# Performance work log

Hardware: AMD Instinct MI355X
Metric: run time of the kernel (lower is better)

Reference implementation:

```python
import jax, jax.numpy as jnp
import numpy as np

B, S, D = 2, 2048, 2048
NH, NKV, HD = 16, 4, 128
ROPE_BASE = 10000.0
NEG = -1e9


def _rope_tables(seq_len, dim):
    inv_freq = 1.0 / ROPE_BASE ** (jnp.arange(0, dim, 2, dtype=jnp.float32) / dim)
    t = jnp.arange(seq_len, dtype=jnp.float32)
    freqs = jnp.outer(t, inv_freq)                      # [S, dim/2]
    return jnp.cos(freqs), jnp.sin(freqs)


def _apply_rope(x, cos, sin):
    # x: [B, S, H, HD]; interleaved-pair rotation matching the original module
    x1 = x[..., ::2]
    x2 = x[..., 1::2]
    c = cos[None, :, None, :]
    s = sin[None, :, None, :]
    out1 = x1 * c - x2 * s
    out2 = x1 * s + x2 * c
    return jnp.stack([out1, out2], axis=-1).reshape(x.shape)


def setup_inputs() -> dict:
    key = jax.random.key(0)
    ks = jax.random.split(key, 5)
    x = jax.random.normal(ks[0], (B, S, D), dtype=jnp.float32)
    # causal additive mask [1, 1, S, S]
    causal = jnp.tril(jnp.ones((S, S), dtype=jnp.bool_))
    mask = jnp.where(causal, 0.0, NEG).astype(jnp.float32)[None, None]
    Wq = jax.random.normal(ks[1], (D, NH * HD), dtype=jnp.float32) * (D ** -0.5)
    Wk = jax.random.normal(ks[2], (D, NKV * HD), dtype=jnp.float32) * (D ** -0.5)
    Wv = jax.random.normal(ks[3], (D, NKV * HD), dtype=jnp.float32) * (D ** -0.5)
    Wo = jax.random.normal(ks[4], (NH * HD, D), dtype=jnp.float32) * ((NH * HD) ** -0.5)
    return {"x": x, "mask": mask, "Wq": Wq, "Wk": Wk, "Wv": Wv, "Wo": Wo}


def reference(x, mask, Wq, Wk, Wv, Wo):
    b, s, _ = x.shape
    q = (x @ Wq).reshape(b, s, NH, HD)
    k = (x @ Wk).reshape(b, s, NKV, HD)
    v = (x @ Wv).reshape(b, s, NKV, HD)

    cos, sin = _rope_tables(s, HD)
    q = _apply_rope(q, cos, sin)
    k = _apply_rope(k, cos, sin)

    rep = NH // NKV
    k = jnp.repeat(k, rep, axis=2)                       # [b, s, NH, HD]
    v = jnp.repeat(v, rep, axis=2)

    q = q.transpose(0, 2, 1, 3)                          # [b, NH, s, HD]
    k = k.transpose(0, 2, 1, 3)
    v = v.transpose(0, 2, 1, 3)

    scores = jnp.einsum('bhqd,bhkd->bhqk', q, k) / jnp.sqrt(jnp.float32(HD))
    scores = scores + mask
    attn = jax.nn.softmax(scores, axis=-1)
    out = jnp.einsum('bhqk,bhkd->bhqd', attn, v)
    out = out.transpose(0, 2, 1, 3).reshape(b, s, NH * HD)
    return out @ Wo
```

## Files before the change

kernel.cpp:

```cpp
#include <hip/hip_runtime.h>
#include <stdint.h>

#define B_    2
#define S_    2048
#define D_    2048
#define NH_   16
#define NKV_  4
#define HD_   128
#define M_    (B_*S_)
#define NQKV_ 3072

typedef __bf16 bf16x8 __attribute__((ext_vector_type(8)));
typedef float  f32x4  __attribute__((ext_vector_type(4)));

__device__ __forceinline__ unsigned short f2bf(float f) {
    unsigned int u = __float_as_uint(f);
    u += 0x7fffu + ((u >> 16) & 1u);
    return (unsigned short)(u >> 16);
}

__device__ __forceinline__ void async_cp16(const unsigned short* g, unsigned short* l) {
    __builtin_amdgcn_global_load_lds((const __attribute__((address_space(1))) void*)g,
                                     (__attribute__((address_space(3))) void*)l, 16, 0, 0);
}

__global__ void cast_x(const float* __restrict__ x, unsigned short* __restrict__ xb) {
    int idx = blockIdx.x * 256 + threadIdx.x;
    float4 v = ((const float4*)x)[idx];
    unsigned int lo = (unsigned int)f2bf(v.x) | ((unsigned int)f2bf(v.y) << 16);
    unsigned int hi = (unsigned int)f2bf(v.z) | ((unsigned int)f2bf(v.w) << 16);
    ((uint2*)xb)[idx] = make_uint2(lo, hi);
}

__global__ void transpose_cast(const float* __restrict__ src,
                               unsigned short* __restrict__ dst, int ncols) {
    __shared__ float tile[32][33];
    int tx = threadIdx.x, ty = threadIdx.y;
    int n0 = blockIdx.x * 32, k0 = blockIdx.y * 32;
#pragma unroll
    for (int i = 0; i < 4; i++) {
        int k = k0 + ty + i * 8;
        tile[ty + i * 8][tx] = src[(long)k * ncols + n0 + tx];
    }
    __syncthreads();
#pragma unroll
    for (int i = 0; i < 4; i++) {
        int n = n0 + ty + i * 8;
        dst[(long)n * 2048 + k0 + tx] = f2bf(tile[tx][ty + i * 8]);
    }
}

__global__ __launch_bounds__(256) void gemm_bt(const unsigned short* __restrict__ A,
                                               const unsigned short* __restrict__ Bt,
                                               float* __restrict__ C, int N, int K) {
    __shared__ unsigned short As[128 * 32];
    __shared__ unsigned short Bs[128 * 32];
    const int tid  = threadIdx.x;
    const int lane = tid & 63, wid = tid >> 6;
    const int quad = lane >> 4, l16 = lane & 15;
    const int wm = wid >> 1, wn = wid & 1;
    const int m0 = blockIdx.y * 128, n0 = blockIdx.x * 128;
    f32x4 acc[4][4] = {};

    for (int k0 = 0; k0 < K; k0 += 32) {
        __syncthreads();
#pragma unroll
        for (int i = 0; i < 2; i++) {
            int gbase = (wid * 2 + i) * 64;
            int g = gbase + lane;
            int row = g >> 2, c = (g & 3) * 8;
            async_cp16(&A[(long)(m0 + row) * K + k0 + c], &As[gbase * 8]);
            async_cp16(&Bt[(long)(n0 + row) * K + k0 + c], &Bs[gbase * 8]);
        }
        __syncthreads();
        bf16x8 af[4], bfr[4];
#pragma unroll
        for (int mt = 0; mt < 4; mt++)
            af[mt] = *(const bf16x8*)&As[(wm * 64 + mt * 16 + l16) * 32 + quad * 8];
#pragma unroll
        for (int nt = 0; nt < 4; nt++)
            bfr[nt] = *(const bf16x8*)&Bs[(wn * 64 + nt * 16 + l16) * 32 + quad * 8];
#pragma unroll
        for (int mt = 0; mt < 4; mt++)
#pragma unroll
            for (int nt = 0; nt < 4; nt++)
                acc[mt][nt] = __builtin_amdgcn_mfma_f32_16x16x32_bf16(af[mt], bfr[nt], acc[mt][nt], 0, 0, 0);
    }
#pragma unroll
    for (int mt = 0; mt < 4; mt++)
#pragma unroll
        for (int nt = 0; nt < 4; nt++)
#pragma unroll
            for (int r = 0; r < 4; r++) {
                long row = m0 + wm * 64 + mt * 16 + quad * 4 + r;
                long col = n0 + wn * 64 + nt * 16 + l16;
                C[row * N + col] = acc[mt][nt][r];
            }
}

__global__ void rope_q(const float* __restrict__ qkv, unsigned short* __restrict__ Qr) {
    int gid = blockIdx.x * 256 + threadIdx.x;
    int p = gid & 63;  int t1 = gid >> 6;
    int h = t1 & 15;   int t2 = t1 >> 4;
    int s = t2 & 2047; int b = t2 >> 11;
    float2 xv = *(const float2*)&qkv[(long)(b * 2048 + s) * 3072 + h * 128 + 2 * p];
    float inv = exp2f(-(float)p * 0.20762050593046014f);
    float ang = (float)s * inv;
    float sn, cs; sincosf(ang, &sn, &cs);
    float o0 = xv.x * cs - xv.y * sn;
    float o1 = xv.x * sn + xv.y * cs;
    unsigned int pk = (unsigned int)f2bf(o0) | ((unsigned int)f2bf(o1) << 16);
    *(unsigned int*)&Qr[(((long)(b * 16 + h) * 2048 + s) * 128) + 2 * p] = pk;
}

__global__ void rope_k(const float* __restrict__ qkv, unsigned short* __restrict__ Kr) {
    int gid = blockIdx.x * 256 + threadIdx.x;
    int p = gid & 63;  int t1 = gid >> 6;
    int kvh = t1 & 3;  int t2 = t1 >> 2;
    int s = t2 & 2047; int b = t2 >> 11;
    float2 xv = *(const float2*)&qkv[(long)(b * 2048 + s) * 3072 + 2048 + kvh * 128 + 2 * p];
    float inv = exp2f(-(float)p * 0.20762050593046014f);
    float ang = (float)s * inv;
    float sn, cs; sincosf(ang, &sn, &cs);
    float o0 = xv.x * cs - xv.y * sn;
    float o1 = xv.x * sn + xv.y * cs;
    unsigned int pk = (unsigned int)f2bf(o0) | ((unsigned int)f2bf(o1) << 16);
    *(unsigned int*)&Kr[(((long)(b * 4 + kvh) * 2048 + s) * 128) + 2 * p] = pk;
}

__global__ void v_trans(const float* __restrict__ qkv, unsigned short* __restrict__ Vt) {
    __shared__ float tile[32][33];
    int tx = threadIdx.x, ty = threadIdx.y;
    int s0 = blockIdx.x * 32, d0 = blockIdx.y * 32;
    int bz = blockIdx.z;
    int b = bz >> 2, kvh = bz & 3;
#pragma unroll
    for (int i = 0; i < 4; i++) {
        int s = s0 + ty + i * 8;
        tile[ty + i * 8][tx] = qkv[(long)(b * 2048 + s) * 3072 + 2560 + kvh * 128 + d0 + tx];
    }
    __syncthreads();
#pragma unroll
    for (int i = 0; i < 4; i++) {
        int d = d0 + ty + i * 8;
        Vt[((long)bz * 128 + d) * 2048 + s0 + tx] = f2bf(tile[tx][ty + i * 8]);
    }
}

__global__ __launch_bounds__(256) void attn_fwd(const unsigned short* __restrict__ Qr,
                                                const unsigned short* __restrict__ Kr,
                                                const unsigned short* __restrict__ Vt,
                                                unsigned short* __restrict__ O) {
    __shared__ unsigned short Ks[64][136];
    __shared__ unsigned short Vs[128][72];
    __shared__ unsigned short Ps[4][16][72];
    const int tid  = threadIdx.x;
    const int lane = tid & 63, wid = tid >> 6;
    const int quad = lane >> 4, l16 = lane & 15;
    const int pid = blockIdx.x, h = blockIdx.y, b = blockIdx.z;
    const int kvh = h >> 2;
    const unsigned short* qp = Qr + (long)(b * NH_ + h) * S_ * HD_;
    const unsigned short* kp = Kr + (long)(b * NKV_ + kvh) * S_ * HD_;
    const unsigned short* vp = Vt + (long)(b * NKV_ + kvh) * HD_ * S_;
    const float sc2 = 0.08838834764831845f * 1.4426950408889634f;

    for (int phase = 0; phase < 2; phase++) {
        const int qt = phase ? pid : 31 - pid;
        const int qw = qt * 64 + wid * 16;

        bf16x8 aq[4];
#pragma unroll
        for (int ks = 0; ks < 4; ks++)
            aq[ks] = *(const bf16x8*)&qp[(long)(qw + l16) * HD_ + ks * 32 + quad * 8];

        f32x4 o[8] = {};
        float mi[4], li[4];
#pragma unroll
        for (int r = 0; r < 4; r++) { mi[r] = -3.0e38f; li[r] = 0.f; }

        for (int kt = 0; kt <= qt; kt++) {
            const int kv0 = kt * 64;
            __syncthreads();
#pragma unroll
            for (int i = 0; i < 4; i++) {
                int idx = tid + i * 256;
                int row = idx >> 4, c = (idx & 15) * 8;
                *(uint4*)&Ks[row][c] = *(const uint4*)&kp[(long)(kv0 + row) * HD_ + c];
            }
#pragma unroll
            for (int i = 0; i < 4; i++) {
                int idx = tid + i * 256;
                int hd = idx >> 3, c = (idx & 7) * 8;
                *(uint4*)&Vs[hd][c] = *(const uint4*)&vp[(long)hd * S_ + kv0 + c];
            }
            __syncthreads();

            f32x4 s[4] = {};
#pragma unroll
            for (int ks = 0; ks < 4; ks++)
#pragma unroll
                for (int nt = 0; nt < 4; nt++) {
                    bf16x8 kb = *(const bf16x8*)&Ks[nt * 16 + l16][ks * 32 + quad * 8];
                    s[nt] = __builtin_amdgcn_mfma_f32_16x16x32_bf16(aq[ks], kb, s[nt], 0, 0, 0);
                }

            float mt[4];
#pragma unroll
            for (int r = 0; r < 4; r++) mt[r] = -3.0e38f;
            if (kv0 + 63 > qw) {
#pragma unroll
                for (int nt = 0; nt < 4; nt++) {
                    int kvp = kv0 + nt * 16 + l16;
#pragma unroll
                    for (int r = 0; r < 4; r++) {
                        float sv = s[nt][r] * sc2;
                        sv = (kvp <= qw + quad * 4 + r) ? sv : -1.0e30f;
                        s[nt][r] = sv;
                        mt[r] = fmaxf(mt[r], sv);
                    }
                }
            } else {
#pragma unroll
                for (int nt = 0; nt < 4; nt++)
#pragma unroll
                    for (int r = 0; r < 4; r++) {
                        float sv = s[nt][r] * sc2;
                        s[nt][r] = sv;
                        mt[r] = fmaxf(mt[r], sv);
                    }
            }
#pragma unroll
            for (int off = 1; off < 16; off <<= 1)
#pragma unroll
                for (int r = 0; r < 4; r++)
                    mt[r] = fmaxf(mt[r], __shfl_xor(mt[r], off));
            float al[4], rs[4];
#pragma unroll
            for (int r = 0; r < 4; r++) {
                float mn = fmaxf(mi[r], mt[r]);
                al[r] = exp2f(mi[r] - mn);
                mi[r] = mn;
                rs[r] = 0.f;
            }
#pragma unroll
            for (int nt = 0; nt < 4; nt++)
#pragma unroll
                for (int r = 0; r < 4; r++) {
                    float pv = exp2f(s[nt][r] - mi[r]);
                    s[nt][r] = pv;
                    rs[r] += pv;
                }
#pragma unroll
            for (int off = 1; off < 16; off <<= 1)
#pragma unroll
                for (int r = 0; r < 4; r++)
                    rs[r] += __shfl_xor(rs[r], off);
#pragma unroll
            for (int r = 0; r < 4; r++) li[r] = li[r] * al[r] + rs[r];
#pragma unroll
            for (int t = 0; t < 8; t++)
#pragma unroll
                for (int r = 0; r < 4; r++) o[t][r] *= al[r];

#pragma unroll
            for (int nt = 0; nt < 4; nt++)
#pragma unroll
                for (int r = 0; r < 4; r++)
                    Ps[wid][quad * 4 + r][nt * 16 + l16] = f2bf(s[nt][r]);

#pragma unroll
            for (int ks2 = 0; ks2 < 2; ks2++) {
                bf16x8 pa = *(const bf16x8*)&Ps[wid][l16][ks2 * 32 + quad * 8];
#pragma unroll
                for (int vt = 0; vt < 8; vt++) {
                    bf16x8 vb = *(const bf16x8*)&Vs[vt * 16 + l16][ks2 * 32 + quad * 8];
                    o[vt] = __builtin_amdgcn_mfma_f32_16x16x32_bf16(pa, vb, o[vt], 0, 0, 0);
                }
            }
        }

#pragma unroll
        for (int r = 0; r < 4; r++) {
            float inv_l = 1.0f / li[r];
            int qpos = qw + quad * 4 + r;
#pragma unroll
            for (int vt = 0; vt < 8; vt++) {
                float val = o[vt][r] * inv_l;
                O[(long)(b * S_ + qpos) * 2048 + h * 128 + vt * 16 + l16] = f2bf(val);
            }
        }
    }
}

extern "C" void kernel_launch(void* const* d_in, const int* in_sizes, int n_in,
                              void* d_out, int out_size, void* d_ws, size_t ws_size,
                              hipStream_t stream) {
    const float* x  = (const float*)d_in[0];
    const float* Wq = (const float*)d_in[2];
    const float* Wk = (const float*)d_in[3];
    const float* Wv = (const float*)d_in[4];
    const float* Wo = (const float*)d_in[5];

    char* ws = (char*)d_ws;
    unsigned short* xb    = (unsigned short*)(ws);
    unsigned short* Wqkvt = (unsigned short*)(ws + 16777216);
    unsigned short* Wot   = (unsigned short*)(ws + 29360128);
    float*          qkv   = (float*)         (ws + 37748736);
    unsigned short* Qr    = (unsigned short*)(ws + 88080384);
    unsigned short* Kr    = (unsigned short*)(ws + 104857600);
    unsigned short* Vt    = (unsigned short*)(ws + 109051904);
    unsigned short* attn  = (unsigned short*)(ws + 113246208);

    cast_x<<<8192, 256, 0, stream>>>(x, xb);
    dim3 tb(32, 8);
    transpose_cast<<<dim3(64, 64), tb, 0, stream>>>(Wq, Wqkvt, 2048);
    transpose_cast<<<dim3(16, 64), tb, 0, stream>>>(Wk, Wqkvt + 2048 * 2048, 512);
    transpose_cast<<<dim3(16, 64), tb, 0, stream>>>(Wv, Wqkvt + 2560 * 2048, 512);
    transpose_cast<<<dim3(64, 64), tb, 0, stream>>>(Wo, Wot, 2048);

    gemm_bt<<<dim3(NQKV_ / 128, M_ / 128), 256, 0, stream>>>(xb, Wqkvt, qkv, NQKV_, D_);

    rope_q<<<16384, 256, 0, stream>>>(qkv, Qr);
    rope_k<<<4096, 256, 0, stream>>>(qkv, Kr);
    v_trans<<<dim3(64, 4, 8), tb, 0, stream>>>(qkv, Vt);

    attn_fwd<<<dim3(16, NH_, B_), 256, 0, stream>>>(Qr, Kr, Vt, attn);

    gemm_bt<<<dim3(D_ / 128, M_ / 128), 256, 0, stream>>>(attn, Wot, (float*)d_out, D_, NH_ * HD_);
}
```

Before: 386.9 us.

## Fuse RoPE and bf16 output into QKV GEMM epilogue, remap grids per XCD

The QKV GEMM epilogue now applies RoPE, using a precomputed cos/sin table and a lane shuffle, and writes bf16 Q/K directly. V is written as a bf16 row-major buffer that a bf16 transpose then reorders. This removes the fp32 qkv intermediate and the separate rope kernels. Both GEMMs use a 1D grid with block-to-tile remapping so adjacent N tiles land on the same XCD for L2 reuse. Attention drops its two-phase paired-tile scheme for one query tile per block on a doubled grid, which trades explicit causal load balancing for more blocks.

```diff
diff --git a/kernel.cpp b/kernel.cpp
--- a/kernel.cpp
+++ b/kernel.cpp
@@ -50,16 +50,33 @@
     }
 }
 
-__global__ __launch_bounds__(256) void gemm_bt(const unsigned short* __restrict__ A,
-                                               const unsigned short* __restrict__ Bt,
-                                               float* __restrict__ C, int N, int K) {
+__global__ void rope_tables(float2* __restrict__ ctab) {
+    int gid = blockIdx.x * 256 + threadIdx.x;
+    int s = gid >> 6, i = gid & 63;
+    float inv = exp2f(-(float)i * 0.20762050593046014f);
+    float ang = (float)s * inv;
+    float sn, cs; sincosf(ang, &sn, &cs);
+    ctab[gid] = make_float2(cs, sn);
+}
+
+__global__ __launch_bounds__(256) void gemm_qkv(const unsigned short* __restrict__ A,
+                                                const unsigned short* __restrict__ Bt,
+                                                const float2* __restrict__ ctab,
+                                                unsigned short* __restrict__ Qr,
+                                                unsigned short* __restrict__ Kr,
+                                                unsigned short* __restrict__ Vrow) {
     __shared__ unsigned short As[128 * 32];
     __shared__ unsigned short Bs[128 * 32];
+    const int K = D_, N = NQKV_;
+    const int bid = blockIdx.x;
+    const int xcd = bid & 7, ii = bid >> 3;
+    const int bx = xcd * 3 + (ii % 3);
+    const int by = ii / 3;
     const int tid  = threadIdx.x;
     const int lane = tid & 63, wid = tid >> 6;
     const int quad = lane >> 4, l16 = lane & 15;
     const int wm = wid >> 1, wn = wid & 1;
-    const int m0 = blockIdx.y * 128, n0 = blockIdx.x * 128;
+    const int m0 = by * 128, n0 = bx * 128;
     f32x4 acc[4][4] = {};
 
     for (int k0 = 0; k0 < K; k0 += 32) {
@@ -86,6 +103,86 @@
             for (int nt = 0; nt < 4; nt++)
                 acc[mt][nt] = __builtin_amdgcn_mfma_f32_16x16x32_bf16(af[mt], bfr[nt], acc[mt][nt], 0, 0, 0);
     }
+
+    if (bx < 20) {
+#pragma unroll
+        for (int mt = 0; mt < 4; mt++)
+#pragma unroll
+            for (int nt = 0; nt < 4; nt++)
+#pragma unroll
+                for (int r = 0; r < 4; r++) {
+                    int row = m0 + wm * 64 + mt * 16 + quad * 4 + r;
+                    int s = row & 2047, b = row >> 11;
+                    int col = n0 + wn * 64 + nt * 16 + l16;
+                    int d = col & 127;
+                    float2 cs = ctab[s * 64 + (d >> 1)];
+                    float own = acc[mt][nt][r];
+                    float other = __shfl_xor(own, 1);
+                    float val = (d & 1) ? (other * cs.y + own * cs.x)
+                                        : (own * cs.x - other * cs.y);
+                    if (col < 2048) {
+                        int h = col >> 7;
+                        Qr[(((long)(b * 16 + h) * 2048 + s) * 128) + d] = f2bf(val);
+                    } else {
+                        int kvh = (col - 2048) >> 7;
+                        Kr[(((long)(b * 4 + kvh) * 2048 + s) * 128) + d] = f2bf(val);
+                    }
+                }
+    } else {
+#pragma unroll
+        for (int mt = 0; mt < 4; mt++)
+#pragma unroll
+            for (int nt = 0; nt < 4; nt++)
+#pragma unroll
+                for (int r = 0; r < 4; r++) {
+                    int row = m0 + wm * 64 + mt * 16 + quad * 4 + r;
+                    int col = n0 + wn * 64 + nt * 16 + l16;
+                    Vrow[(long)row * 512 + (col - 2560)] = f2bf(acc[mt][nt][r]);
+                }
+    }
+}
+
+__global__ __launch_bounds__(256) void gemm_bt(const unsigned short* __restrict__ A,
+                                               const unsigned short* __restrict__ Bt,
+                                               float* __restrict__ C, int N, int K,
+                                               int nbxl) {
+    __shared__ unsigned short As[128 * 32];
+    __shared__ unsigned short Bs[128 * 32];
+    const int bid = blockIdx.x;
+    const int xcd = bid & 7, ii = bid >> 3;
+    const int bx = xcd * nbxl + (ii % nbxl);
+    const int by = ii / nbxl;
+    const int tid  = threadIdx.x;
+    const int lane = tid & 63, wid = tid >> 6;
+    const int quad = lane >> 4, l16 = lane & 15;
+    const int wm = wid >> 1, wn = wid & 1;
+    const int m0 = by * 128, n0 = bx * 128;
+    f32x4 acc[4][4] = {};
+
+    for (int k0 = 0; k0 < K; k0 += 32) {
+        __syncthreads();
+#pragma unroll
+        for (int i = 0; i < 2; i++) {
+            int gbase = (wid * 2 + i) * 64;
+            int g = gbase + lane;
+            int row = g >> 2, c = (g & 3) * 8;
+            async_cp16(&A[(long)(m0 + row) * K + k0 + c], &As[gbase * 8]);
+            async_cp16(&Bt[(long)(n0 + row) * K + k0 + c], &Bs[gbase * 8]);
+        }
+        __syncthreads();
+        bf16x8 af[4], bfr[4];
+#pragma unroll
+        for (int mt = 0; mt < 4; mt++)
+            af[mt] = *(const bf16x8*)&As[(wm * 64 + mt * 16 + l16) * 32 + quad * 8];
+#pragma unroll
+        for (int nt = 0; nt < 4; nt++)
+            bfr[nt] = *(const bf16x8*)&Bs[(wn * 64 + nt * 16 + l16) * 32 + quad * 8];
+#pragma unroll
+        for (int mt = 0; mt < 4; mt++)
+#pragma unroll
+            for (int nt = 0; nt < 4; nt++)
+                acc[mt][nt] = __builtin_amdgcn_mfma_f32_16x16x32_bf16(af[mt], bfr[nt], acc[mt][nt], 0, 0, 0);
+    }
 #pragma unroll
     for (int mt = 0; mt < 4; mt++)
 #pragma unroll
@@ -98,38 +195,9 @@
             }
 }
 
-__global__ void rope_q(const float* __restrict__ qkv, unsigned short* __restrict__ Qr) {
-    int gid = blockIdx.x * 256 + threadIdx.x;
-    int p = gid & 63;  int t1 = gid >> 6;
-    int h = t1 & 15;   int t2 = t1 >> 4;
-    int s = t2 & 2047; int b = t2 >> 11;
-    float2 xv = *(const float2*)&qkv[(long)(b * 2048 + s) * 3072 + h * 128 + 2 * p];
-    float inv = exp2f(-(float)p * 0.20762050593046014f);
-    float ang = (float)s * inv;
-    float sn, cs; sincosf(ang, &sn, &cs);
-    float o0 = xv.x * cs - xv.y * sn;
-    float o1 = xv.x * sn + xv.y * cs;
-    unsigned int pk = (unsigned int)f2bf(o0) | ((unsigned int)f2bf(o1) << 16);
-    *(unsigned int*)&Qr[(((long)(b * 16 + h) * 2048 + s) * 128) + 2 * p] = pk;
-}
-
-__global__ void rope_k(const float* __restrict__ qkv, unsigned short* __restrict__ Kr) {
-    int gid = blockIdx.x * 256 + threadIdx.x;
-    int p = gid & 63;  int t1 = gid >> 6;
-    int kvh = t1 & 3;  int t2 = t1 >> 2;
-    int s = t2 & 2047; int b = t2 >> 11;
-    float2 xv = *(const float2*)&qkv[(long)(b * 2048 + s) * 3072 + 2048 + kvh * 128 + 2 * p];
-    float inv = exp2f(-(float)p * 0.20762050593046014f);
-    float ang = (float)s * inv;
-    float sn, cs; sincosf(ang, &sn, &cs);
-    float o0 = xv.x * cs - xv.y * sn;
-    float o1 = xv.x * sn + xv.y * cs;
-    unsigned int pk = (unsigned int)f2bf(o0) | ((unsigned int)f2bf(o1) << 16);
-    *(unsigned int*)&Kr[(((long)(b * 4 + kvh) * 2048 + s) * 128) + 2 * p] = pk;
-}
-
-__global__ void v_trans(const float* __restrict__ qkv, unsigned short* __restrict__ Vt) {
-    __shared__ float tile[32][33];
+__global__ void v_trans_bf(const unsigned short* __restrict__ Vrow,
+                           unsigned short* __restrict__ Vt) {
+    __shared__ unsigned short tile[32][34];
     int tx = threadIdx.x, ty = threadIdx.y;
     int s0 = blockIdx.x * 32, d0 = blockIdx.y * 32;
     int bz = blockIdx.z;
@@ -137,13 +205,13 @@
 #pragma unroll
     for (int i = 0; i < 4; i++) {
         int s = s0 + ty + i * 8;
-        tile[ty + i * 8][tx] = qkv[(long)(b * 2048 + s) * 3072 + 2560 + kvh * 128 + d0 + tx];
+        tile[ty + i * 8][tx] = Vrow[(long)(b * 2048 + s) * 512 + kvh * 128 + d0 + tx];
     }
     __syncthreads();
 #pragma unroll
     for (int i = 0; i < 4; i++) {
         int d = d0 + ty + i * 8;
-        Vt[((long)bz * 128 + d) * 2048 + s0 + tx] = f2bf(tile[tx][ty + i * 8]);
+        Vt[((long)bz * 128 + d) * 2048 + s0 + tx] = tile[tx][ty + i * 8];
     }
 }
 
@@ -157,137 +225,134 @@
     const int tid  = threadIdx.x;
     const int lane = tid & 63, wid = tid >> 6;
     const int quad = lane >> 4, l16 = lane & 15;
-    const int pid = blockIdx.x, h = blockIdx.y, b = blockIdx.z;
+    const int qt = 31 - blockIdx.x;
+    const int h = blockIdx.y, b = blockIdx.z;
     const int kvh = h >> 2;
+    const int qw = qt * 64 + wid * 16;
     const unsigned short* qp = Qr + (long)(b * NH_ + h) * S_ * HD_;
     const unsigned short* kp = Kr + (long)(b * NKV_ + kvh) * S_ * HD_;
     const unsigned short* vp = Vt + (long)(b * NKV_ + kvh) * HD_ * S_;
     const float sc2 = 0.08838834764831845f * 1.4426950408889634f;
 
-    for (int phase = 0; phase < 2; phase++) {
-        const int qt = phase ? pid : 31 - pid;
-        const int qw = qt * 64 + wid * 16;
-
-        bf16x8 aq[4];
+    bf16x8 aq[4];
+#pragma unroll
+    for (int ks = 0; ks < 4; ks++)
+        aq[ks] = *(const bf16x8*)&qp[(long)(qw + l16) * HD_ + ks * 32 + quad * 8];
+
+    f32x4 o[8] = {};
+    float mi[4], li[4];
+#pragma unroll
+    for (int r = 0; r < 4; r++) { mi[r] = -3.0e38f; li[r] = 0.f; }
+
+    for (int kt = 0; kt <= qt; kt++) {
+        const int kv0 = kt * 64;
+        __syncthreads();
+#pragma unroll
+        for (int i = 0; i < 4; i++) {
+            int idx = tid + i * 256;
+            int row = idx >> 4, c = (idx & 15) * 8;
+            *(uint4*)&Ks[row][c] = *(const uint4*)&kp[(long)(kv0 + row) * HD_ + c];
+        }
+#pragma unroll
+        for (int i = 0; i < 4; i++) {
+            int idx = tid + i * 256;
+            int hd = idx >> 3, c = (idx & 7) * 8;
+            *(uint4*)&Vs[hd][c] = *(const uint4*)&vp[(long)hd * S_ + kv0 + c];
+        }
+        __syncthreads();
+
+        f32x4 s[4] = {};
 #pragma unroll
         for (int ks = 0; ks < 4; ks++)
-            aq[ks] = *(const bf16x8*)&qp[(long)(qw + l16) * HD_ + ks * 32 + quad * 8];
-
-        f32x4 o[8] = {};
-        float mi[4], li[4];
-#pragma unroll
-        for (int r = 0; r < 4; r++) { mi[r] = -3.0e38f; li[r] = 0.f; }
-
-        for (int kt = 0; kt <= qt; kt++) {
-            const int kv0 = kt * 64;
-            __syncthreads();
-#pragma unroll
-            for (int i = 0; i < 4; i++) {
-                int idx = tid + i * 256;
-                int row = idx >> 4, c = (idx & 15) * 8;
-                *(uint4*)&Ks[row][c] = *(const uint4*)&kp[(long)(kv0 + row) * HD_ + c];
-            }
-#pragma unroll
-            for (int i = 0; i < 4; i++) {
-                int idx = tid + i * 256;
-                int hd = idx >> 3, c = (idx & 7) * 8;
-                *(uint4*)&Vs[hd][c] = *(const uint4*)&vp[(long)hd * S_ + kv0 + c];
-            }
-            __syncthreads();
-
-            f32x4 s[4] = {};
-#pragma unroll
-            for (int ks = 0; ks < 4; ks++)
-#pragma unroll
-                for (int nt = 0; nt < 4; nt++) {
-                    bf16x8 kb = *(const bf16x8*)&Ks[nt * 16 + l16][ks * 32 + quad * 8];
-                    s[nt] = __builtin_amdgcn_mfma_f32_16x16x32_bf16(aq[ks], kb, s[nt], 0, 0, 0);
+#pragma unroll
+            for (int nt = 0; nt < 4; nt++) {
+                bf16x8 kb = *(const bf16x8*)&Ks[nt * 16 + l16][ks * 32 + quad * 8];
+                s[nt] = __builtin_amdgcn_mfma_f32_16x16x32_bf16(aq[ks], kb, s[nt], 0, 0, 0);
+            }
+
+        float mt[4];
+#pragma unroll
+        for (int r = 0; r < 4; r++) mt[r] = -3.0e38f;
+        if (kv0 + 63 > qw) {
+#pragma unroll
+            for (int nt = 0; nt < 4; nt++) {
+                int kvp = kv0 + nt * 16 + l16;
+#pragma unroll
+                for (int r = 0; r < 4; r++) {
+                    float sv = s[nt][r] * sc2;
+                    sv = (kvp <= qw + quad * 4 + r) ? sv : -1.0e30f;
+                    s[nt][r] = sv;
+                    mt[r] = fmaxf(mt[r], sv);
                 }
-
-            float mt[4];
-#pragma unroll
-            for (int r = 0; r < 4; r++) mt[r] = -3.0e38f;
-            if (kv0 + 63 > qw) {
-#pragma unroll
-                for (int nt = 0; nt < 4; nt++) {
-                    int kvp = kv0 + nt * 16 + l16;
-#pragma unroll
-                    for (int r = 0; r < 4; r++) {
-                        float sv = s[nt][r] * sc2;
-                        sv = (kvp <= qw + quad * 4 + r) ? sv : -1.0e30f;
-                        s[nt][r] = sv;
-                        mt[r] = fmaxf(mt[r], sv);
-                    }
+            }
+        } else {
+#pragma unroll
+            for (int nt = 0; nt < 4; nt++)
+#pragma unroll
+                for (int r = 0; r < 4; r++) {
+                    float sv = s[nt][r] * sc2;
+                    s[nt][r] = sv;
+                    mt[r] = fmaxf(mt[r], sv);
                 }
-            } else {
-#pragma unroll
-                for (int nt = 0; nt < 4; nt++)
-#pragma unroll
-                    for (int r = 0; r < 4; r++) {
-                        float sv = s[nt][r] * sc2;
-                        s[nt][r] = sv;
-                        mt[r] = fmaxf(mt[r], sv);
-                    }
-            }
-#pragma unroll
-            for (int off = 1; off < 16; off <<= 1)
-#pragma unroll
-                for (int r = 0; r < 4; r++)
-                    mt[r] = fmaxf(mt[r], __shfl_xor(mt[r], off));
-            float al[4], rs[4];
+        }
+#pragma unroll
+        for (int off = 1; off < 16; off <<= 1)
+#pragma unroll
+            for (int r = 0; r < 4; r++)
+                mt[r] = fmaxf(mt[r], __shfl_xor(mt[r], off));
+        float al[4], rs[4];
+#pragma unroll
+        for (int r = 0; r < 4; r++) {
+            float mn = fmaxf(mi[r], mt[r]);
+            al[r] = exp2f(mi[r] - mn);
+            mi[r] = mn;
+            rs[r] = 0.f;
+        }
+#pragma unroll
+        for (int nt = 0; nt < 4; nt++)
 #pragma unroll
             for (int r = 0; r < 4; r++) {
-                float mn = fmaxf(mi[r], mt[r]);
-                al[r] = exp2f(mi[r] - mn);
-                mi[r] = mn;
-                rs[r] = 0.f;
-            }
-#pragma unroll
-            for (int nt = 0; nt < 4; nt++)
-#pragma unroll
-                for (int r = 0; r < 4; r++) {
-                    float pv = exp2f(s[nt][r] - mi[r]);
-                    s[nt][r] = pv;
-                    rs[r] += pv;
-                }
-#pragma unroll
-            for (int off = 1; off < 16; off <<= 1)
-#pragma unroll
-                for (int r = 0; r < 4; r++)
-                    rs[r] += __shfl_xor(rs[r], off);
-#pragma unroll
-            for (int r = 0; r < 4; r++) li[r] = li[r] * al[r] + rs[r];
-#pragma unroll
-            for (int t = 0; t < 8; t++)
-#pragma unroll
-                for (int r = 0; r < 4; r++) o[t][r] *= al[r];
-
-#pragma unroll
-            for (int nt = 0; nt < 4; nt++)
-#pragma unroll
-                for (int r = 0; r < 4; r++)
-                    Ps[wid][quad * 4 + r][nt * 16 + l16] = f2bf(s[nt][r]);
-
-#pragma unroll
-            for (int ks2 = 0; ks2 < 2; ks2++) {
-                bf16x8 pa = *(const bf16x8*)&Ps[wid][l16][ks2 * 32 + quad * 8];
-#pragma unroll
-                for (int vt = 0; vt < 8; vt++) {
-                    bf16x8 vb = *(const bf16x8*)&Vs[vt * 16 + l16][ks2 * 32 + quad * 8];
-                    o[vt] = __builtin_amdgcn_mfma_f32_16x16x32_bf16(pa, vb, o[vt], 0, 0, 0);
-                }
-            }
-        }
-
-#pragma unroll
-        for (int r = 0; r < 4; r++) {
-            float inv_l = 1.0f / li[r];
-            int qpos = qw + quad * 4 + r;
+                float pv = exp2f(s[nt][r] - mi[r]);
+                s[nt][r] = pv;
+                rs[r] += pv;
+            }
+#pragma unroll
+        for (int off = 1; off < 16; off <<= 1)
+#pragma unroll
+            for (int r = 0; r < 4; r++)
+                rs[r] += __shfl_xor(rs[r], off);
+#pragma unroll
+        for (int r = 0; r < 4; r++) li[r] = li[r] * al[r] + rs[r];
+#pragma unroll
+        for (int t = 0; t < 8; t++)
+#pragma unroll
+            for (int r = 0; r < 4; r++) o[t][r] *= al[r];
+
+#pragma unroll
+        for (int nt = 0; nt < 4; nt++)
+#pragma unroll
+            for (int r = 0; r < 4; r++)
+                Ps[wid][quad * 4 + r][nt * 16 + l16] = f2bf(s[nt][r]);
+
+#pragma unroll
+        for (int ks2 = 0; ks2 < 2; ks2++) {
+            bf16x8 pa = *(const bf16x8*)&Ps[wid][l16][ks2 * 32 + quad * 8];
 #pragma unroll
             for (int vt = 0; vt < 8; vt++) {
-                float val = o[vt][r] * inv_l;
-                O[(long)(b * S_ + qpos) * 2048 + h * 128 + vt * 16 + l16] = f2bf(val);
-            }
+                bf16x8 vb = *(const bf16x8*)&Vs[vt * 16 + l16][ks2 * 32 + quad * 8];
+                o[vt] = __builtin_amdgcn_mfma_f32_16x16x32_bf16(pa, vb, o[vt], 0, 0, 0);
+            }
+        }
+    }
+
+#pragma unroll
+    for (int r = 0; r < 4; r++) {
+        float inv_l = 1.0f / li[r];
+        int qpos = qw + quad * 4 + r;
+#pragma unroll
+        for (int vt = 0; vt < 8; vt++) {
+            float val = o[vt][r] * inv_l;
+            O[(long)(b * S_ + qpos) * 2048 + h * 128 + vt * 16 + l16] = f2bf(val);
         }
     }
 }
@@ -305,11 +370,12 @@
     unsigned short* xb    = (unsigned short*)(ws);
     unsigned short* Wqkvt = (unsigned short*)(ws + 16777216);
     unsigned short* Wot   = (unsigned short*)(ws + 29360128);
-    float*          qkv   = (float*)         (ws + 37748736);
-    unsigned short* Qr    = (unsigned short*)(ws + 88080384);
-    unsigned short* Kr    = (unsigned short*)(ws + 104857600);
-    unsigned short* Vt    = (unsigned short*)(ws + 109051904);
-    unsigned short* attn  = (unsigned short*)(ws + 113246208);
+    float2*         ctab  = (float2*)        (ws + 37748736);
+    unsigned short* Qr    = (unsigned short*)(ws + 38797312);
+    unsigned short* Kr    = (unsigned short*)(ws + 55574528);
+    unsigned short* Vrow  = (unsigned short*)(ws + 59768832);
+    unsigned short* Vt    = (unsigned short*)(ws + 63963136);
+    unsigned short* attn  = (unsigned short*)(ws + 68157440);
 
     cast_x<<<8192, 256, 0, stream>>>(x, xb);
     dim3 tb(32, 8);
@@ -317,14 +383,13 @@
     transpose_cast<<<dim3(16, 64), tb, 0, stream>>>(Wk, Wqkvt + 2048 * 2048, 512);
     transpose_cast<<<dim3(16, 64), tb, 0, stream>>>(Wv, Wqkvt + 2560 * 2048, 512);
     transpose_cast<<<dim3(64, 64), tb, 0, stream>>>(Wo, Wot, 2048);
-
-    gemm_bt<<<dim3(NQKV_ / 128, M_ / 128), 256, 0, stream>>>(xb, Wqkvt, qkv, NQKV_, D_);
-
-    rope_q<<<16384, 256, 0, stream>>>(qkv, Qr);
-    rope_k<<<4096, 256, 0, stream>>>(qkv, Kr);
-    v_trans<<<dim3(64, 4, 8), tb, 0, stream>>>(qkv, Vt);
-
-    attn_fwd<<<dim3(16, NH_, B_), 256, 0, stream>>>(Qr, Kr, Vt, attn);
-
-    gemm_bt<<<dim3(D_ / 128, M_ / 128), 256, 0, stream>>>(attn, Wot, (float*)d_out, D_, NH_ * HD_);
-}
+    rope_tables<<<512, 256, 0, stream>>>(ctab);
+
+    gemm_qkv<<<24 * 32, 256, 0, stream>>>(xb, Wqkvt, ctab, Qr, Kr, Vrow);
+
+    v_trans_bf<<<dim3(64, 4, 8), tb, 0, stream>>>(Vrow, Vt);
+
+    attn_fwd<<<dim3(32, NH_, B_), 256, 0, stream>>>(Qr, Kr, Vt, attn);
+
+    gemm_bt<<<16 * 32, 256, 0, stream>>>(attn, Wot, (float*)d_out, D_, NH_ * HD_, 2);
+}
```

After: 550.8 us. 42.4% more time.
